# Kernel optimization log

Measured on AMD Instinct MI355X. Metric: run time of the kernel, lower is better.

Reference implementation:

```python
import jax, jax.numpy as jnp
import numpy as np
from jax import lax

BN_EPS = 1e-5


def _bn(t, g, b, m, v):
    # eval-mode BatchNorm2d over channel axis 1
    scale = (g / jnp.sqrt(v + BN_EPS))[None, :, None, None]
    return (t - m[None, :, None, None]) * scale + b[None, :, None, None]


def _conv1x1(t, w):
    # w: (out_c, in_c)
    return jnp.einsum('bchw,oc->bohw', t, w)


def setup_inputs() -> dict:
    key = jax.random.key(0)
    ks = jax.random.split(key, 8)
    B, C_in, H, W = 16, 640, 32, 32
    x = jax.random.normal(ks[0], (B, C_in, H, W), dtype=jnp.float32)

    def bn_params(k, c):
        k1, k2, k3, k4 = jax.random.split(k, 4)
        return (jax.random.normal(k1, (c,), jnp.float32) * 0.1 + 1.0,  # gamma
                jax.random.normal(k2, (c,), jnp.float32) * 0.1,        # beta
                jax.random.normal(k3, (c,), jnp.float32) * 0.1,        # running mean
                jax.random.uniform(k4, (c,), jnp.float32) + 0.5)       # running var

    bn1_g, bn1_b, bn1_m, bn1_v = bn_params(ks[1], 640)
    w_in = jax.random.normal(ks[2], (64, 640), jnp.float32) / np.sqrt(640)
    bnin_g, bnin_b, bnin_m, bnin_v = bn_params(ks[3], 64)
    w_emb = jax.random.normal(ks[4], (640, 1664), jnp.float32) / np.sqrt(1664)
    bne_g, bne_b, bne_m, bne_v = bn_params(ks[5], 640)
    w_out = jax.random.normal(ks[6], (640, 640), jnp.float32) / np.sqrt(640)
    bno_g, bno_b, bno_m, bno_v = bn_params(ks[7], 640)

    return dict(x=x,
                bn1_g=bn1_g, bn1_b=bn1_b, bn1_m=bn1_m, bn1_v=bn1_v,
                w_in=w_in, bnin_g=bnin_g, bnin_b=bnin_b, bnin_m=bnin_m, bnin_v=bnin_v,
                w_emb=w_emb, bne_g=bne_g, bne_b=bne_b, bne_m=bne_m, bne_v=bne_v,
                w_out=w_out, bno_g=bno_g, bno_b=bno_b, bno_m=bno_m, bno_v=bno_v)


def reference(x,
              bn1_g, bn1_b, bn1_m, bn1_v,
              w_in, bnin_g, bnin_b, bnin_m, bnin_v,
              w_emb, bne_g, bne_b, bne_m, bne_v,
              w_out, bno_g, bno_b, bno_m, bno_v):
    KH, KW = 5, 5
    x = jax.nn.relu(_bn(x, bn1_g, bn1_b, bn1_m, bn1_v))
    x = jax.nn.relu(_bn(_conv1x1(x, w_in), bnin_g, bnin_b, bnin_m, bnin_v))
    x0 = jax.nn.relu(x)  # second ReLU in original forward (no-op but faithful)
    # F.normalize(x, dim=1, p=2), eps=1e-12 (PyTorch default)
    norm = jnp.sqrt(jnp.sum(x0 * x0, axis=1, keepdims=True))
    identity = x0 / jnp.maximum(norm, 1e-12)
    b, c, h, w = identity.shape
    # unfold: (b, c*KH*KW, h, w), channel-major ordering matches torch Unfold
    patches = lax.conv_general_dilated_patches(
        identity, (KH, KW), (1, 1), ((2, 2), (2, 2)))
    corr = patches.reshape(b, c, KH * KW, h, w) * identity[:, :, None, :, :]
    corr = corr.reshape(b, c * KH * KW, h, w)
    # featureL2Norm: sqrt(sum(x^2, 1) + 1e-6)
    gs = corr / jnp.sqrt(jnp.sum(corr * corr, axis=1, keepdims=True) + 1e-6)
    feat = jnp.concatenate([identity, gs], axis=1)  # (b, 1664, h, w)
    e = jax.nn.relu(_bn(_conv1x1(feat, w_emb), bne_g, bne_b, bne_m, bne_v))
    out = _bn(_conv1x1(e, w_out), bno_g, bno_b, bno_m, bno_v)
    # dropout in eval mode = identity
    return out
```

## Files before the change

kernel.cpp:

```cpp
#include <hip/hip_runtime.h>
#include <math.h>

#define BN_EPS 1e-5f

using short8  = __attribute__((ext_vector_type(8))) short;
using f32x16  = __attribute__((ext_vector_type(16))) float;


__device__ __forceinline__ float bflo(unsigned u) { return __uint_as_float(u << 16); }
__device__ __forceinline__ float bfhi(unsigned u) { return __uint_as_float(u & 0xffff0000u); }

__device__ __forceinline__ unsigned bf16_rne(float f) {
    unsigned u = __float_as_uint(f);
    return (u + 0x7fffu + ((u >> 16) & 1u)) >> 16;
}
__device__ __forceinline__ unsigned pack_bf16(float lo, float hi) {
    return bf16_rne(lo) | (bf16_rne(hi) << 16);
}
__device__ __forceinline__ unsigned pk_hu(float lo, float hi) {
    unsigned a = __float_as_uint(lo) + 0x8000u;
    unsigned b = __float_as_uint(hi) + 0x8000u;
    return __builtin_amdgcn_perm(b, a, 0x07060302u);
}
__device__ __forceinline__ unsigned pmul_fast(unsigned a, unsigned b) {
    return pk_hu(bflo(a) * bflo(b), bfhi(a) * bfhi(b));
}

__global__ __launch_bounds__(256)
void k_prepAll(const float* __restrict__ g1, const float* __restrict__ b1,
               const float* __restrict__ m1, const float* __restrict__ v1,
               const float* __restrict__ w_in,
               const float* __restrict__ gi, const float* __restrict__ bi,
               const float* __restrict__ mi, const float* __restrict__ vi,
               const float* __restrict__ w_emb,
               const float* __restrict__ ge, const float* __restrict__ be,
               const float* __restrict__ me, const float* __restrict__ ve,
               const float* __restrict__ w_out,
               const float* __restrict__ go, const float* __restrict__ bo,
               const float* __restrict__ mo, const float* __restrict__ vo,
               float* __restrict__ s1, float* __restrict__ b1c,
               float* __restrict__ biasI, float* __restrict__ biasE, float* __restrict__ biasO,
               unsigned* __restrict__ wIt, unsigned* __restrict__ wEt, unsigned* __restrict__ wOt)
{
    __shared__ float row[1664];
    const int tid = threadIdx.x;

    if (blockIdx.x < 640) {
        const int oc = blockIdx.x;
#pragma unroll
        for (int it = 0; it < 2; it++) {
            int u = it * 256 + tid;
            if (u < 416)
                ((float4*)row)[u] = ((const float4*)&w_emb[(size_t)oc * 1664])[u];
        }
        __syncthreads();
        if (tid < 208) {
            int kc = tid >> 2, kh = (tid >> 1) & 1, ksub = tid & 1;
            int k0 = kc * 32 + kh * 16 + ksub * 8;
            float sc = ge[oc] * rsqrtf(ve[oc] + BN_EPS);
            float v[8];
#pragma unroll
            for (int j = 0; j < 8; j++) {
                int kgp = k0 + j;
                int orig;
                if (kgp < 64) orig = kgp;
                else { int t = kgp - 64; orig = 64 + (t & 63) * 25 + (t >> 6); }
                v[j] = row[orig] * sc;
            }
            int mt = oc >> 7, mf = (oc >> 5) & 3;
            int idx = (mt * 52 + kc) * 512 + (mf * 2 + kh) * 64 + ksub * 32 + (oc & 31);
            ((uint4*)wEt)[idx] = make_uint4(pack_bf16(v[0], v[1]), pack_bf16(v[2], v[3]),
                                            pack_bf16(v[4], v[5]), pack_bf16(v[6], v[7]));
        }
        return;
    }

    int i = (blockIdx.x - 640) * 256 + tid;

    if (i < 640) {
        float s = g1[i] * rsqrtf(v1[i] + BN_EPS);
        s1[i] = s; b1c[i] = b1[i] - m1[i] * s;
    } else if (i < 704) {
        int c = i - 640;
        float s = gi[c] * rsqrtf(vi[c] + BN_EPS);
        biasI[c] = bi[c] - mi[c] * s;
    } else if (i < 1344) {
        int c = i - 704;
        float s = ge[c] * rsqrtf(ve[c] + BN_EPS);
        biasE[c] = be[c] - me[c] * s;
    } else if (i < 1984) {
        int c = i - 1344;
        float s = go[c] * rsqrtf(vo[c] + BN_EPS);
        biasO[c] = bo[c] - mo[c] * s;
    }

    if (i >= 2048 && i < 7168) {
        int u = i - 2048;
        int kc = u >> 8, w = u & 255;
        int mf = w >> 7, kh = (w >> 6) & 1, sl = w & 63;
        int oc = mf * 32 + (sl & 31);
        int k0 = kc * 32 + kh * 16 + (sl >> 5) * 8;
        float sc = gi[oc] * rsqrtf(vi[oc] + BN_EPS);
        unsigned d[4];
#pragma unroll
        for (int q = 0; q < 4; q++)
            d[q] = pack_bf16(w_in[oc * 640 + k0 + 2 * q] * sc,
                             w_in[oc * 640 + k0 + 2 * q + 1] * sc);
        ((uint4*)wIt)[u] = make_uint4(d[0], d[1], d[2], d[3]);
    }

    if (i >= 8192 && i < 59392) {
        int u = i - 8192;
        int ci = u >> 9, w = u & 511;
        int mt = ci / 20, kc = ci - mt * 20;
        int mf = w >> 7, kh = (w >> 6) & 1, sl = w & 63;
        int oc = mt * 128 + mf * 32 + (sl & 31);
        int k0 = kc * 32 + kh * 16 + (sl >> 5) * 8;
        float sc = go[oc] * rsqrtf(vo[oc] + BN_EPS);
        unsigned d[4];
#pragma unroll
        for (int q = 0; q < 4; q++)
            d[q] = pack_bf16(w_out[oc * 640 + k0 + 2 * q] * sc,
                             w_out[oc * 640 + k0 + 2 * q + 1] * sc);
        ((uint4*)wOt)[u] = make_uint4(d[0], d[1], d[2], d[3]);
    }
}

__global__ __launch_bounds__(512, 1)
void k_identity(const float* __restrict__ x,
                const float* __restrict__ s1, const float* __restrict__ b1c,
                const unsigned* __restrict__ wIt, const float* __restrict__ biasI,
                unsigned* __restrict__ ident)
{
    __shared__ short smem[2][4096];
    __shared__ float Tpart[64 * 65];
    __shared__ float T[64 * 68];
    __shared__ float inv[64];

    const int tid  = threadIdx.x;
    const int half = tid >> 8;
    const int t    = tid & 255;
    const int l = t & 63, wv = t >> 6;
    const int mf = wv >> 1, nf = wv & 1;
    const int p0 = blockIdx.x * 64;
    const int b = p0 >> 10, hw0 = p0 & 1023;

    f32x16 acc;
#pragma unroll
    for (int r = 0; r < 16; r++) acc[r] = 0.f;

    for (int i = 0; i < 10; i++) {
        const int kc = half * 10 + i;
        uint4 av = ((const uint4*)wIt)[kc * 256 + t];
        int bnf = t >> 7, bkh = (t >> 6) & 1, sl = t & 63;
        int px = bnf * 32 + (sl & 31);
        int ch0 = kc * 32 + bkh * 16 + (sl >> 5) * 8;
        float4 sA = *(const float4*)&s1[ch0], sB = *(const float4*)&s1[ch0 + 4];
        float4 bA = *(const float4*)&b1c[ch0], bB = *(const float4*)&b1c[ch0 + 4];
        float vv[8];
        const float* xp = &x[((size_t)b * 640 + ch0) * 1024 + hw0 + px];
        vv[0] = fmaxf(fmaf(xp[0], sA.x, bA.x), 0.f);
        vv[1] = fmaxf(fmaf(xp[1024], sA.y, bA.y), 0.f);
        vv[2] = fmaxf(fmaf(xp[2048], sA.z, bA.z), 0.f);
        vv[3] = fmaxf(fmaf(xp[3072], sA.w, bA.w), 0.f);
        vv[4] = fmaxf(fmaf(xp[4096], sB.x, bB.x), 0.f);
        vv[5] = fmaxf(fmaf(xp[5120], sB.y, bB.y), 0.f);
        vv[6] = fmaxf(fmaf(xp[6144], sB.z, bB.z), 0.f);
        vv[7] = fmaxf(fmaf(xp[7168], sB.w, bB.w), 0.f);
        uint4 bvpk = make_uint4(pack_bf16(vv[0], vv[1]), pack_bf16(vv[2], vv[3]),
                                pack_bf16(vv[4], vv[5]), pack_bf16(vv[6], vv[7]));
        __syncthreads();
        ((uint4*)smem[half])[t] = av;
        ((uint4*)(smem[half] + 2048))[t] = bvpk;
        __syncthreads();
#pragma unroll
        for (int kh = 0; kh < 2; kh++) {
            short8 a  = *(const short8*)&smem[half][((mf * 2 + kh) * 64 + l) * 8];
            short8 bb = *(const short8*)&smem[half][2048 + ((nf * 2 + kh) * 64 + l) * 8];
            acc = __builtin_amdgcn_mfma_f32_32x32x16_bf16(a, bb, acc, 0, 0, 0);
        }
    }
    if (half == 1) {
#pragma unroll
        for (int r = 0; r < 16; r++) {
            int m = mf * 32 + (r & 3) + 8 * (r >> 2) + 4 * (l >> 5);
            int px = nf * 32 + (l & 31);
            Tpart[px * 65 + m] = acc[r];
        }
    }
    __syncthreads();
    if (half == 0) {
#pragma unroll
        for (int r = 0; r < 16; r++) {
            int m = mf * 32 + (r & 3) + 8 * (r >> 2) + 4 * (l >> 5);
            int px = nf * 32 + (l & 31);
            float v = acc[r] + Tpart[px * 65 + m];
            T[px * 68 + m] = fmaxf(v + biasI[m], 0.f);
        }
    }
    __syncthreads();
    if (tid < 64) {
        float sum = 0.f;
#pragma unroll 8
        for (int c = 0; c < 64; c++) { float v = T[tid * 68 + c]; sum = fmaf(v, v, sum); }
        inv[tid] = 1.f / fmaxf(sqrtf(sum), 1e-12f);
    }
    __syncthreads();
    {
        int px = tid >> 3, q = tid & 7;
        float iv = inv[px];
        unsigned d[4];
#pragma unroll
        for (int t2 = 0; t2 < 4; t2++)
            d[t2] = pack_bf16(T[px * 68 + q * 8 + 2 * t2] * iv,
                              T[px * 68 + q * 8 + 2 * t2 + 1] * iv);
        *(uint4*)&ident[(size_t)(p0 + px) * 32 + q * 4] = make_uint4(d[0], d[1], d[2], d[3]);
    }
}

__device__ __forceinline__ uint4 gen_feat_unit(const short* slab, const short* ctrs,
                                               int kcAbs, int t)
{
    const int hf = t >> 7, sl = t & 63;
    const int bkh = (t >> 6) & 1;
    const int cl = bkh * 16 + (sl >> 5) * 8;
    if (kcAbs < 2) {
        int spxC = (hf + 2) * 36 + (sl & 31) + 2;
        return *(const uint4*)&slab[spxC * 72 + kcAbs * 32 + cl];
    } else {
        int pxl = hf * 32 + (sl & 31);
        int idx = kcAbs - 2;
        int ksp = idx >> 1;
        int cb = (idx & 1) * 32 + cl;
        int kho = ksp / 5, kwo = ksp - kho * 5;
        int spx = (hf + kho) * 36 + (sl & 31) + kwo;
        const unsigned* nb = (const unsigned*)&slab[spx * 72 + cb];
        const unsigned* ct = (const unsigned*)&ctrs[pxl * 72 + cb];
        return make_uint4(pmul_fast(nb[0], ct[0]), pmul_fast(nb[1], ct[1]),
                          pmul_fast(nb[2], ct[2]), pmul_fast(nb[3], ct[3]));
    }
}

__global__ __launch_bounds__(640, 1)
void k_fused(const unsigned* __restrict__ ident,
             const unsigned* __restrict__ wEt, const float* __restrict__ biasE,
             const unsigned* __restrict__ wOt, const float* __restrict__ biasO,
             float* __restrict__ out)
{
    __shared__ short slab[15552];
    __shared__ short ctrs[4608];
    __shared__ float invDs[64];
    __shared__ char  stg[2][16384];
    __shared__ uint4 Ep[20 * 256];

    const int tid = threadIdx.x;
    const int l = tid & 63;
    const int w = tid >> 6;
    const int mt = w >> 1, mf0 = (w & 1) * 2;
    const int pt = blockIdx.x;
    const int b = pt >> 4, r0 = (pt & 15) * 2;

#pragma unroll
    for (int it = 0; it < 3; it++) {
        int u = it * 640 + tid;
        if (u < 1728) {
            int spx = u >> 3, q = u & 7;
            int sr = spx / 36, sc = spx - sr * 36;
            int r = r0 + sr - 2, cc = sc - 2;
            uint4 v = make_uint4(0u, 0u, 0u, 0u);
            if (r >= 0 && r < 32 && cc >= 0 && cc < 32)
                v = *(const uint4*)&ident[((size_t)(b * 1024 + r * 32 + cc) * 64 + q * 8) / 2];
            *(uint4*)&slab[spx * 72 + q * 8] = v;
        }
    }
    __syncthreads();

    if (tid < 512) {
        int px = tid >> 3, part = tid & 7;
        int rh = px >> 5, rw = px & 31;
        float ctr[8];
        const unsigned* cp = (const unsigned*)&slab[((rh + 2) * 36 + rw + 2) * 72 + part * 8];
#pragma unroll
        for (int d = 0; d < 4; d++) { ctr[2 * d] = bflo(cp[d]); ctr[2 * d + 1] = bfhi(cp[d]); }
        float sum = 0.f;
#pragma unroll
        for (int k = 0; k < 25; k++) {
            const int kh = k / 5, kw = k % 5;
            const unsigned* nb = (const unsigned*)&slab[((rh + kh) * 36 + rw + kw) * 72 + part * 8];
#pragma unroll
            for (int d = 0; d < 4; d++) {
                float q0 = bflo(nb[d]) * ctr[2 * d];
                float q1 = bfhi(nb[d]) * ctr[2 * d + 1];
                sum = fmaf(q0, q0, sum); sum = fmaf(q1, q1, sum);
            }
        }
        sum += __shfl_xor(sum, 1);
        sum += __shfl_xor(sum, 2);
        sum += __shfl_xor(sum, 4);
        if (part == 0) invDs[px] = rsqrtf(sum + 1e-6f);
    }
    __syncthreads();

    if (tid < 512) {
        int px = tid >> 3, q = tid & 7;
        int spx = ((px >> 5) + 2) * 36 + (px & 31) + 2;
        const unsigned* src = (const unsigned*)&slab[spx * 72 + q * 8];
        float iv = invDs[px];
        unsigned d[4];
#pragma unroll
        for (int dd = 0; dd < 4; dd++)
            d[dd] = pk_hu(bflo(src[dd]) * iv, bfhi(src[dd]) * iv);
        *(uint4*)&ctrs[px * 72 + q * 8] = make_uint4(d[0], d[1], d[2], d[3]);
    }
    __syncthreads();

    const uint4* A = (const uint4*)wEt + (size_t)(mt * 52) * 512;
    const bool has2 = (tid < 384);

    f32x16 acc[2][2];
#pragma unroll
    for (int i = 0; i < 2; i++)
#pragma unroll
        for (int j = 0; j < 2; j++)
#pragma unroll
            for (int r = 0; r < 16; r++) acc[i][j][r] = 0.f;

    {
        uint4 f = gen_feat_unit(slab, ctrs, (tid >> 8), tid & 255);
        *(uint4*)&stg[0][tid * 16] = f;
        if (has2) {
            int u = tid + 640;
            uint4 f2 = gen_feat_unit(slab, ctrs, (u >> 8), u & 255);
            *(uint4*)&stg[0][u * 16] = f2;
        }
    }
    __syncthreads();

    for (int c = 0; c < 13; c++) {
        const int cur = c & 1, nxt = cur ^ 1;
        if (c < 12) {
            int kc0 = (c + 1) * 4;
            uint4 f = gen_feat_unit(slab, ctrs, kc0 + (tid >> 8), tid & 255);
            *(uint4*)&stg[nxt][tid * 16] = f;
            if (has2) {
                int u = tid + 640;
                uint4 f2 = gen_feat_unit(slab, ctrs, kc0 + (u >> 8), u & 255);
                *(uint4*)&stg[nxt][u * 16] = f2;
            }
        }
#pragma unroll
        for (int kcL = 0; kcL < 4; kcL++) {
            const int kc = c * 4 + kcL;
            uint4 av[2][2], bv[2][2];
#pragma unroll
            for (int mi = 0; mi < 2; mi++)
#pragma unroll
                for (int kh = 0; kh < 2; kh++)
                    av[mi][kh] = A[(size_t)kc * 512 + (((mf0 + mi) * 2 + kh) << 6) + l];
#pragma unroll
            for (int ni = 0; ni < 2; ni++)
#pragma unroll
                for (int kh = 0; kh < 2; kh++)
                    bv[ni][kh] = *(const uint4*)&stg[cur][(kcL * 256 + (ni << 7) + (kh << 6) + l) * 16];
#pragma unroll
            for (int kh = 0; kh < 2; kh++) {
                acc[0][0] = __builtin_amdgcn_mfma_f32_32x32x16_bf16(*(short8*)&av[0][kh], *(short8*)&bv[0][kh], acc[0][0], 0, 0, 0);
                acc[0][1] = __builtin_amdgcn_mfma_f32_32x32x16_bf16(*(short8*)&av[0][kh], *(short8*)&bv[1][kh], acc[0][1], 0, 0, 0);
                acc[1][0] = __builtin_amdgcn_mfma_f32_32x32x16_bf16(*(short8*)&av[1][kh], *(short8*)&bv[0][kh], acc[1][0], 0, 0, 0);
                acc[1][1] = __builtin_amdgcn_mfma_f32_32x32x16_bf16(*(short8*)&av[1][kh], *(short8*)&bv[1][kh], acc[1][1], 0, 0, 0);
            }
        }
        __syncthreads();
    }

#pragma unroll
    for (int mi = 0; mi < 2; mi++) {
        const int kbase = (w * 2 + mi) * 256;
#pragma unroll
        for (int ni = 0; ni < 2; ni++) {
#pragma unroll
            for (int rg = 0; rg < 4; rg++) {
                int ocb = w * 64 + mi * 32 + 8 * rg + 4 * (l >> 5);
                float4 bb = *(const float4*)&biasE[ocb];
                unsigned d0 = pack_bf16(fmaxf(acc[mi][ni][rg * 4 + 0] + bb.x, 0.f),
                                        fmaxf(acc[mi][ni][rg * 4 + 1] + bb.y, 0.f));
                unsigned d1 = pack_bf16(fmaxf(acc[mi][ni][rg * 4 + 2] + bb.z, 0.f),
                                        fmaxf(acc[mi][ni][rg * 4 + 3] + bb.w, 0.f));
                int unit = kbase + (ni << 7) + ((rg >> 1) << 6) + ((rg & 1) << 5) + (l & 31);
                ((uint2*)Ep)[unit * 2 + (l >> 5)] = make_uint2(d0, d1);
            }
        }
    }
    __syncthreads();

    const int p0 = pt * 64;
    const int hw0 = p0 & 1023;
    const uint4* Ao = (const uint4*)wOt + (size_t)(mt * 20) * 512;

    f32x16 acc2[2][2];
#pragma unroll
    for (int i = 0; i < 2; i++)
#pragma unroll
        for (int j = 0; j < 2; j++)
#pragma unroll
            for (int r = 0; r < 16; r++) acc2[i][j][r] = 0.f;

#pragma unroll 2
    for (int kc = 0; kc < 20; kc++) {
        uint4 av[2][2], bv[2][2];
#pragma unroll
        for (int mi = 0; mi < 2; mi++)
#pragma unroll
            for (int kh = 0; kh < 2; kh++)
                av[mi][kh] = Ao[(size_t)kc * 512 + (((mf0 + mi) * 2 + kh) << 6) + l];
#pragma unroll
        for (int ni = 0; ni < 2; ni++)
#pragma unroll
            for (int kh = 0; kh < 2; kh++)
                bv[ni][kh] = Ep[kc * 256 + (ni << 7) + (kh << 6) + l];
#pragma unroll
        for (int kh = 0; kh < 2; kh++) {
            acc2[0][0] = __builtin_amdgcn_mfma_f32_32x32x16_bf16(*(short8*)&av[0][kh], *(short8*)&bv[0][kh], acc2[0][0], 0, 0, 0);
            acc2[0][1] = __builtin_amdgcn_mfma_f32_32x32x16_bf16(*(short8*)&av[0][kh], *(short8*)&bv[1][kh], acc2[0][1], 0, 0, 0);
            acc2[1][0] = __builtin_amdgcn_mfma_f32_32x32x16_bf16(*(short8*)&av[1][kh], *(short8*)&bv[0][kh], acc2[1][0], 0, 0, 0);
            acc2[1][1] = __builtin_amdgcn_mfma_f32_32x32x16_bf16(*(short8*)&av[1][kh], *(short8*)&bv[1][kh], acc2[1][1], 0, 0, 0);
        }
    }

#pragma unroll
    for (int mi = 0; mi < 2; mi++)
#pragma unroll
        for (int ni = 0; ni < 2; ni++) {
            int pxl = ni * 32 + (l & 31);
#pragma unroll
            for (int r = 0; r < 16; r++) {
                int oc = w * 64 + mi * 32 + (r & 3) + 8 * (r >> 2) + 4 * (l >> 5);
                out[((size_t)b * 640 + oc) * 1024 + hw0 + pxl] = acc2[mi][ni][r] + biasO[oc];
            }
        }
}

extern "C" void kernel_launch(void* const* d_in, const int* in_sizes, int n_in,
                              void* d_out, int out_size, void* d_ws, size_t ws_size,
                              hipStream_t stream)
{
    const float* x    = (const float*)d_in[0];
    const float* g1   = (const float*)d_in[1];
    const float* b1   = (const float*)d_in[2];
    const float* m1   = (const float*)d_in[3];
    const float* v1   = (const float*)d_in[4];
    const float* w_in = (const float*)d_in[5];
    const float* gi   = (const float*)d_in[6];
    const float* bi   = (const float*)d_in[7];
    const float* mi   = (const float*)d_in[8];
    const float* vi   = (const float*)d_in[9];
    const float* w_emb= (const float*)d_in[10];
    const float* ge   = (const float*)d_in[11];
    const float* be   = (const float*)d_in[12];
    const float* me   = (const float*)d_in[13];
    const float* ve   = (const float*)d_in[14];
    const float* w_out= (const float*)d_in[15];
    const float* go   = (const float*)d_in[16];
    const float* bo   = (const float*)d_in[17];
    const float* mo   = (const float*)d_in[18];
    const float* vo   = (const float*)d_in[19];

    char* ws = (char*)d_ws;
    float*    s1    = (float*)(ws + 0);
    float*    b1c   = (float*)(ws + 2560);
    float*    biasI = (float*)(ws + 5120);
    float*    biasE = (float*)(ws + 5376);
    float*    biasO = (float*)(ws + 7936);
    unsigned* wIt   = (unsigned*)(ws + 16384);
    unsigned* wOt   = (unsigned*)(ws + 98304);
    unsigned* wEt   = (unsigned*)(ws + 917504);
    unsigned* ident = (unsigned*)(ws + 3047424);
    float*    out   = (float*)d_out;

    k_prepAll<<<872, 256, 0, stream>>>(g1, b1, m1, v1, w_in, gi, bi, mi, vi,
                                       w_emb, ge, be, me, ve, w_out, go, bo, mo, vo,
                                       s1, b1c, biasI, biasE, biasO, wIt, wEt, wOt);
    k_identity<<<256, 512, 0, stream>>>(x, s1, b1c, wIt, biasI, ident);
    k_fused<<<256, 640, 0, stream>>>(ident, wEt, biasE, wOt, biasO, out);
}
```

Before: 195.6 us.

## Halve fused-kernel pixel tile to one row, doubling grid to 512 blocks

The fused correlation+embedding+output kernel now processes one image row (32 pixels) per block instead of two rows, launching 512 blocks. Shared memory and accumulators shrink, and launch bounds allow several blocks per CU. This targets the MI355X's 256 CUs being only one block deep, trading better occupancy and latency hiding for halved weight reuse (each weight tile is read twice as often) and higher halo overhead in the slab load.

```diff
diff --git a/kernel.cpp b/kernel.cpp
--- a/kernel.cpp
+++ b/kernel.cpp
@@ -218,52 +218,51 @@
     }
 }
 
-__device__ __forceinline__ uint4 gen_feat_unit(const short* slab, const short* ctrs,
-                                               int kcAbs, int t)
+__device__ __forceinline__ uint4 gen_feat_unit32(const short* slab, const short* ctrs,
+                                                 int kcAbs, int t)
 {
-    const int hf = t >> 7, sl = t & 63;
+    const int sl = t & 63;
     const int bkh = (t >> 6) & 1;
+    const int px = sl & 31;
     const int cl = bkh * 16 + (sl >> 5) * 8;
     if (kcAbs < 2) {
-        int spxC = (hf + 2) * 36 + (sl & 31) + 2;
-        return *(const uint4*)&slab[spxC * 72 + kcAbs * 32 + cl];
+        return *(const uint4*)&slab[(2 * 36 + px + 2) * 72 + kcAbs * 32 + cl];
     } else {
-        int pxl = hf * 32 + (sl & 31);
         int idx = kcAbs - 2;
         int ksp = idx >> 1;
         int cb = (idx & 1) * 32 + cl;
         int kho = ksp / 5, kwo = ksp - kho * 5;
-        int spx = (hf + kho) * 36 + (sl & 31) + kwo;
+        int spx = kho * 36 + px + kwo;
         const unsigned* nb = (const unsigned*)&slab[spx * 72 + cb];
-        const unsigned* ct = (const unsigned*)&ctrs[pxl * 72 + cb];
+        const unsigned* ct = (const unsigned*)&ctrs[px * 72 + cb];
         return make_uint4(pmul_fast(nb[0], ct[0]), pmul_fast(nb[1], ct[1]),
                           pmul_fast(nb[2], ct[2]), pmul_fast(nb[3], ct[3]));
     }
 }
 
-__global__ __launch_bounds__(640, 1)
+__global__ __launch_bounds__(640, 5)
 void k_fused(const unsigned* __restrict__ ident,
              const unsigned* __restrict__ wEt, const float* __restrict__ biasE,
              const unsigned* __restrict__ wOt, const float* __restrict__ biasO,
              float* __restrict__ out)
 {
-    __shared__ short slab[15552];
-    __shared__ short ctrs[4608];
-    __shared__ float invDs[64];
-    __shared__ char  stg[2][16384];
-    __shared__ uint4 Ep[20 * 256];
+    __shared__ short slab[180 * 72];
+    __shared__ short ctrs[32 * 72];
+    __shared__ float invDs[32];
+    __shared__ char  stg[2][4096];
+    __shared__ uint4 Ep[20 * 128];
 
     const int tid = threadIdx.x;
     const int l = tid & 63;
     const int w = tid >> 6;
     const int mt = w >> 1, mf0 = (w & 1) * 2;
-    const int pt = blockIdx.x;
-    const int b = pt >> 4, r0 = (pt & 15) * 2;
+    const int b = blockIdx.x >> 5;
+    const int r0 = blockIdx.x & 31;
 
 #pragma unroll
     for (int it = 0; it < 3; it++) {
         int u = it * 640 + tid;
-        if (u < 1728) {
+        if (u < 1440) {
             int spx = u >> 3, q = u & 7;
             int sr = spx / 36, sc = spx - sr * 36;
             int r = r0 + sr - 2, cc = sc - 2;
@@ -275,18 +274,17 @@
     }
     __syncthreads();
 
-    if (tid < 512) {
+    if (tid < 256) {
         int px = tid >> 3, part = tid & 7;
-        int rh = px >> 5, rw = px & 31;
         float ctr[8];
-        const unsigned* cp = (const unsigned*)&slab[((rh + 2) * 36 + rw + 2) * 72 + part * 8];
+        const unsigned* cp = (const unsigned*)&slab[(2 * 36 + px + 2) * 72 + part * 8];
 #pragma unroll
         for (int d = 0; d < 4; d++) { ctr[2 * d] = bflo(cp[d]); ctr[2 * d + 1] = bfhi(cp[d]); }
         float sum = 0.f;
 #pragma unroll
         for (int k = 0; k < 25; k++) {
             const int kh = k / 5, kw = k % 5;
-            const unsigned* nb = (const unsigned*)&slab[((rh + kh) * 36 + rw + kw) * 72 + part * 8];
+            const unsigned* nb = (const unsigned*)&slab[(kh * 36 + px + kw) * 72 + part * 8];
 #pragma unroll
             for (int d = 0; d < 4; d++) {
                 float q0 = bflo(nb[d]) * ctr[2 * d];
@@ -301,10 +299,9 @@
     }
     __syncthreads();
 
-    if (tid < 512) {
+    if (tid < 256) {
         int px = tid >> 3, q = tid & 7;
-        int spx = ((px >> 5) + 2) * 36 + (px & 31) + 2;
-        const unsigned* src = (const unsigned*)&slab[spx * 72 + q * 8];
+        const unsigned* src = (const unsigned*)&slab[(2 * 36 + px + 2) * 72 + q * 8];
         float iv = invDs[px];
         unsigned d[4];
 #pragma unroll
@@ -315,59 +312,42 @@
     __syncthreads();
 
     const uint4* A = (const uint4*)wEt + (size_t)(mt * 52) * 512;
-    const bool has2 = (tid < 384);
-
-    f32x16 acc[2][2];
+
+    f32x16 acc[2];
 #pragma unroll
     for (int i = 0; i < 2; i++)
 #pragma unroll
-        for (int j = 0; j < 2; j++)
-#pragma unroll
-            for (int r = 0; r < 16; r++) acc[i][j][r] = 0.f;
-
-    {
-        uint4 f = gen_feat_unit(slab, ctrs, (tid >> 8), tid & 255);
+        for (int r = 0; r < 16; r++) acc[i][r] = 0.f;
+
+    if (tid < 256) {
+        uint4 f = gen_feat_unit32(slab, ctrs, tid >> 7, tid & 127);
         *(uint4*)&stg[0][tid * 16] = f;
-        if (has2) {
-            int u = tid + 640;
-            uint4 f2 = gen_feat_unit(slab, ctrs, (u >> 8), u & 255);
-            *(uint4*)&stg[0][u * 16] = f2;
-        }
-    }
-    __syncthreads();
-
-    for (int c = 0; c < 13; c++) {
+    }
+    __syncthreads();
+
+    for (int c = 0; c < 26; c++) {
         const int cur = c & 1, nxt = cur ^ 1;
-        if (c < 12) {
-            int kc0 = (c + 1) * 4;
-            uint4 f = gen_feat_unit(slab, ctrs, kc0 + (tid >> 8), tid & 255);
+        if (c < 25 && tid < 256) {
+            int kc0 = (c + 1) * 2;
+            uint4 f = gen_feat_unit32(slab, ctrs, kc0 + (tid >> 7), tid & 127);
             *(uint4*)&stg[nxt][tid * 16] = f;
-            if (has2) {
-                int u = tid + 640;
-                uint4 f2 = gen_feat_unit(slab, ctrs, kc0 + (u >> 8), u & 255);
-                *(uint4*)&stg[nxt][u * 16] = f2;
-            }
-        }
-#pragma unroll
-        for (int kcL = 0; kcL < 4; kcL++) {
-            const int kc = c * 4 + kcL;
-            uint4 av[2][2], bv[2][2];
+        }
+#pragma unroll
+        for (int kcL = 0; kcL < 2; kcL++) {
+            const int kc = c * 2 + kcL;
+            uint4 av[2][2], bv[2];
 #pragma unroll
             for (int mi = 0; mi < 2; mi++)
 #pragma unroll
                 for (int kh = 0; kh < 2; kh++)
                     av[mi][kh] = A[(size_t)kc * 512 + (((mf0 + mi) * 2 + kh) << 6) + l];
 #pragma unroll
-            for (int ni = 0; ni < 2; ni++)
-#pragma unroll
-                for (int kh = 0; kh < 2; kh++)
-                    bv[ni][kh] = *(const uint4*)&stg[cur][(kcL * 256 + (ni << 7) + (kh << 6) + l) * 16];
+            for (int kh = 0; kh < 2; kh++)
+                bv[kh] = *(const uint4*)&stg[cur][(kcL * 128 + (kh << 6) + l) * 16];
 #pragma unroll
             for (int kh = 0; kh < 2; kh++) {
-                acc[0][0] = __builtin_amdgcn_mfma_f32_32x32x16_bf16(*(short8*)&av[0][kh], *(short8*)&bv[0][kh], acc[0][0], 0, 0, 0);
-                acc[0][1] = __builtin_amdgcn_mfma_f32_32x32x16_bf16(*(short8*)&av[0][kh], *(short8*)&bv[1][kh], acc[0][1], 0, 0, 0);
-                acc[1][0] = __builtin_amdgcn_mfma_f32_32x32x16_bf16(*(short8*)&av[1][kh], *(short8*)&bv[0][kh], acc[1][0], 0, 0, 0);
-                acc[1][1] = __builtin_amdgcn_mfma_f32_32x32x16_bf16(*(short8*)&av[1][kh], *(short8*)&bv[1][kh], acc[1][1], 0, 0, 0);
+                acc[0] = __builtin_amdgcn_mfma_f32_32x32x16_bf16(*(short8*)&av[0][kh], *(short8*)&bv[kh], acc[0], 0, 0, 0);
+                acc[1] = __builtin_amdgcn_mfma_f32_32x32x16_bf16(*(short8*)&av[1][kh], *(short8*)&bv[kh], acc[1], 0, 0, 0);
             }
         }
         __syncthreads();
@@ -375,69 +355,57 @@
 
 #pragma unroll
     for (int mi = 0; mi < 2; mi++) {
-        const int kbase = (w * 2 + mi) * 256;
-#pragma unroll
-        for (int ni = 0; ni < 2; ni++) {
-#pragma unroll
-            for (int rg = 0; rg < 4; rg++) {
-                int ocb = w * 64 + mi * 32 + 8 * rg + 4 * (l >> 5);
-                float4 bb = *(const float4*)&biasE[ocb];
-                unsigned d0 = pack_bf16(fmaxf(acc[mi][ni][rg * 4 + 0] + bb.x, 0.f),
-                                        fmaxf(acc[mi][ni][rg * 4 + 1] + bb.y, 0.f));
-                unsigned d1 = pack_bf16(fmaxf(acc[mi][ni][rg * 4 + 2] + bb.z, 0.f),
-                                        fmaxf(acc[mi][ni][rg * 4 + 3] + bb.w, 0.f));
-                int unit = kbase + (ni << 7) + ((rg >> 1) << 6) + ((rg & 1) << 5) + (l & 31);
-                ((uint2*)Ep)[unit * 2 + (l >> 5)] = make_uint2(d0, d1);
-            }
-        }
-    }
-    __syncthreads();
-
-    const int p0 = pt * 64;
-    const int hw0 = p0 & 1023;
+        const int kbase = (w * 2 + mi) * 128;
+#pragma unroll
+        for (int rg = 0; rg < 4; rg++) {
+            int ocb = w * 64 + mi * 32 + 8 * rg + 4 * (l >> 5);
+            float4 bb = *(const float4*)&biasE[ocb];
+            unsigned d0 = pack_bf16(fmaxf(acc[mi][rg * 4 + 0] + bb.x, 0.f),
+                                    fmaxf(acc[mi][rg * 4 + 1] + bb.y, 0.f));
+            unsigned d1 = pack_bf16(fmaxf(acc[mi][rg * 4 + 2] + bb.z, 0.f),
+                                    fmaxf(acc[mi][rg * 4 + 3] + bb.w, 0.f));
+            int unit = kbase + ((rg >> 1) << 6) + ((rg & 1) << 5) + (l & 31);
+            ((uint2*)Ep)[unit * 2 + (l >> 5)] = make_uint2(d0, d1);
+        }
+    }
+    __syncthreads();
+
+    const int hw0 = r0 * 32;
     const uint4* Ao = (const uint4*)wOt + (size_t)(mt * 20) * 512;
 
-    f32x16 acc2[2][2];
+    f32x16 acc2[2];
 #pragma unroll
     for (int i = 0; i < 2; i++)
 #pragma unroll
-        for (int j = 0; j < 2; j++)
-#pragma unroll
-            for (int r = 0; r < 16; r++) acc2[i][j][r] = 0.f;
+        for (int r = 0; r < 16; r++) acc2[i][r] = 0.f;
 
 #pragma unroll 2
     for (int kc = 0; kc < 20; kc++) {
-        uint4 av[2][2], bv[2][2];
+        uint4 av[2][2], bv[2];
 #pragma unroll
         for (int mi = 0; mi < 2; mi++)
 #pragma unroll
             for (int kh = 0; kh < 2; kh++)
                 av[mi][kh] = Ao[(size_t)kc * 512 + (((mf0 + mi) * 2 + kh) << 6) + l];
 #pragma unroll
-        for (int ni = 0; ni < 2; ni++)
-#pragma unroll
-            for (int kh = 0; kh < 2; kh++)
-                bv[ni][kh] = Ep[kc * 256 + (ni << 7) + (kh << 6) + l];
+        for (int kh = 0; kh < 2; kh++)
+            bv[kh] = Ep[kc * 128 + (kh << 6) + l];
 #pragma unroll
         for (int kh = 0; kh < 2; kh++) {
-            acc2[0][0] = __builtin_amdgcn_mfma_f32_32x32x16_bf16(*(short8*)&av[0][kh], *(short8*)&bv[0][kh], acc2[0][0], 0, 0, 0);
-            acc2[0][1] = __builtin_amdgcn_mfma_f32_32x32x16_bf16(*(short8*)&av[0][kh], *(short8*)&bv[1][kh], acc2[0][1], 0, 0, 0);
-            acc2[1][0] = __builtin_amdgcn_mfma_f32_32x32x16_bf16(*(short8*)&av[1][kh], *(short8*)&bv[0][kh], acc2[1][0], 0, 0, 0);
-            acc2[1][1] = __builtin_amdgcn_mfma_f32_32x32x16_bf16(*(short8*)&av[1][kh], *(short8*)&bv[1][kh], acc2[1][1], 0, 0, 0);
-        }
-    }
-
-#pragma unroll
-    for (int mi = 0; mi < 2; mi++)
-#pragma unroll
-        for (int ni = 0; ni < 2; ni++) {
-            int pxl = ni * 32 + (l & 31);
-#pragma unroll
-            for (int r = 0; r < 16; r++) {
-                int oc = w * 64 + mi * 32 + (r & 3) + 8 * (r >> 2) + 4 * (l >> 5);
-                out[((size_t)b * 640 + oc) * 1024 + hw0 + pxl] = acc2[mi][ni][r] + biasO[oc];
-            }
-        }
+            acc2[0] = __builtin_amdgcn_mfma_f32_32x32x16_bf16(*(short8*)&av[0][kh], *(short8*)&bv[kh], acc2[0], 0, 0, 0);
+            acc2[1] = __builtin_amdgcn_mfma_f32_32x32x16_bf16(*(short8*)&av[1][kh], *(short8*)&bv[kh], acc2[1], 0, 0, 0);
+        }
+    }
+
+#pragma unroll
+    for (int mi = 0; mi < 2; mi++) {
+        int px = l & 31;
+#pragma unroll
+        for (int r = 0; r < 16; r++) {
+            int oc = w * 64 + mi * 32 + (r & 3) + 8 * (r >> 2) + 4 * (l >> 5);
+            out[((size_t)b * 640 + oc) * 1024 + hw0 + px] = acc2[mi][r] + biasO[oc];
+        }
+    }
 }
 
 extern "C" void kernel_launch(void* const* d_in, const int* in_sizes, int n_in,
@@ -481,5 +449,5 @@
                                        w_emb, ge, be, me, ve, w_out, go, bo, mo, vo,
                                        s1, b1c, biasI, biasE, biasO, wIt, wEt, wOt);
     k_identity<<<256, 512, 0, stream>>>(x, s1, b1c, wIt, biasI, ident);
-    k_fused<<<256, 640, 0, stream>>>(ident, wEt, biasE, wOt, biasO, out);
-}
+    k_fused<<<512, 640, 0, stream>>>(ident, wEt, biasE, wOt, biasO, out);
+}
```

After: 221.8 us. 1.13x slower.

## Fuse identity computation into main kernel with halo recompute

Applied to the files above, without the earlier changes.

Removes the separate k_identity kernel and the ident buffer round-trip. Each block of the fused kernel now computes BN+ReLU, the 640->64 conv, ReLU and L2 normalization for its 216-pixel halo slab directly from x using MFMA, and writes the result into shared memory. This saves one launch and the global write/read of the intermediate, but recomputes halo rows (216 vs 64 pixels per block, roughly 3.4x the identity work) and reads x with strided per-channel loads. Launch bounds were also changed to request 3 waves per EU.

```diff
diff --git a/kernel.cpp b/kernel.cpp
--- a/kernel.cpp
+++ b/kernel.cpp
@@ -123,98 +123,6 @@
             d[q] = pack_bf16(w_out[oc * 640 + k0 + 2 * q] * sc,
                              w_out[oc * 640 + k0 + 2 * q + 1] * sc);
         ((uint4*)wOt)[u] = make_uint4(d[0], d[1], d[2], d[3]);
-    }
-}
-
-__global__ __launch_bounds__(512, 1)
-void k_identity(const float* __restrict__ x,
-                const float* __restrict__ s1, const float* __restrict__ b1c,
-                const unsigned* __restrict__ wIt, const float* __restrict__ biasI,
-                unsigned* __restrict__ ident)
-{
-    __shared__ short smem[2][4096];
-    __shared__ float Tpart[64 * 65];
-    __shared__ float T[64 * 68];
-    __shared__ float inv[64];
-
-    const int tid  = threadIdx.x;
-    const int half = tid >> 8;
-    const int t    = tid & 255;
-    const int l = t & 63, wv = t >> 6;
-    const int mf = wv >> 1, nf = wv & 1;
-    const int p0 = blockIdx.x * 64;
-    const int b = p0 >> 10, hw0 = p0 & 1023;
-
-    f32x16 acc;
-#pragma unroll
-    for (int r = 0; r < 16; r++) acc[r] = 0.f;
-
-    for (int i = 0; i < 10; i++) {
-        const int kc = half * 10 + i;
-        uint4 av = ((const uint4*)wIt)[kc * 256 + t];
-        int bnf = t >> 7, bkh = (t >> 6) & 1, sl = t & 63;
-        int px = bnf * 32 + (sl & 31);
-        int ch0 = kc * 32 + bkh * 16 + (sl >> 5) * 8;
-        float4 sA = *(const float4*)&s1[ch0], sB = *(const float4*)&s1[ch0 + 4];
-        float4 bA = *(const float4*)&b1c[ch0], bB = *(const float4*)&b1c[ch0 + 4];
-        float vv[8];
-        const float* xp = &x[((size_t)b * 640 + ch0) * 1024 + hw0 + px];
-        vv[0] = fmaxf(fmaf(xp[0], sA.x, bA.x), 0.f);
-        vv[1] = fmaxf(fmaf(xp[1024], sA.y, bA.y), 0.f);
-        vv[2] = fmaxf(fmaf(xp[2048], sA.z, bA.z), 0.f);
-        vv[3] = fmaxf(fmaf(xp[3072], sA.w, bA.w), 0.f);
-        vv[4] = fmaxf(fmaf(xp[4096], sB.x, bB.x), 0.f);
-        vv[5] = fmaxf(fmaf(xp[5120], sB.y, bB.y), 0.f);
-        vv[6] = fmaxf(fmaf(xp[6144], sB.z, bB.z), 0.f);
-        vv[7] = fmaxf(fmaf(xp[7168], sB.w, bB.w), 0.f);
-        uint4 bvpk = make_uint4(pack_bf16(vv[0], vv[1]), pack_bf16(vv[2], vv[3]),
-                                pack_bf16(vv[4], vv[5]), pack_bf16(vv[6], vv[7]));
-        __syncthreads();
-        ((uint4*)smem[half])[t] = av;
-        ((uint4*)(smem[half] + 2048))[t] = bvpk;
-        __syncthreads();
-#pragma unroll
-        for (int kh = 0; kh < 2; kh++) {
-            short8 a  = *(const short8*)&smem[half][((mf * 2 + kh) * 64 + l) * 8];
-            short8 bb = *(const short8*)&smem[half][2048 + ((nf * 2 + kh) * 64 + l) * 8];
-            acc = __builtin_amdgcn_mfma_f32_32x32x16_bf16(a, bb, acc, 0, 0, 0);
-        }
-    }
-    if (half == 1) {
-#pragma unroll
-        for (int r = 0; r < 16; r++) {
-            int m = mf * 32 + (r & 3) + 8 * (r >> 2) + 4 * (l >> 5);
-            int px = nf * 32 + (l & 31);
-            Tpart[px * 65 + m] = acc[r];
-        }
-    }
-    __syncthreads();
-    if (half == 0) {
-#pragma unroll
-        for (int r = 0; r < 16; r++) {
-            int m = mf * 32 + (r & 3) + 8 * (r >> 2) + 4 * (l >> 5);
-            int px = nf * 32 + (l & 31);
-            float v = acc[r] + Tpart[px * 65 + m];
-            T[px * 68 + m] = fmaxf(v + biasI[m], 0.f);
-        }
-    }
-    __syncthreads();
-    if (tid < 64) {
-        float sum = 0.f;
-#pragma unroll 8
-        for (int c = 0; c < 64; c++) { float v = T[tid * 68 + c]; sum = fmaf(v, v, sum); }
-        inv[tid] = 1.f / fmaxf(sqrtf(sum), 1e-12f);
-    }
-    __syncthreads();
-    {
-        int px = tid >> 3, q = tid & 7;
-        float iv = inv[px];
-        unsigned d[4];
-#pragma unroll
-        for (int t2 = 0; t2 < 4; t2++)
-            d[t2] = pack_bf16(T[px * 68 + q * 8 + 2 * t2] * iv,
-                              T[px * 68 + q * 8 + 2 * t2 + 1] * iv);
-        *(uint4*)&ident[(size_t)(p0 + px) * 32 + q * 4] = make_uint4(d[0], d[1], d[2], d[3]);
     }
 }
 
@@ -241,14 +149,16 @@
     }
 }
 
-__global__ __launch_bounds__(640, 1)
-void k_fused(const unsigned* __restrict__ ident,
-             const unsigned* __restrict__ wEt, const float* __restrict__ biasE,
-             const unsigned* __restrict__ wOt, const float* __restrict__ biasO,
-             float* __restrict__ out)
+__global__ __launch_bounds__(640, 3)
+void k_mega(const float* __restrict__ x,
+            const float* __restrict__ s1, const float* __restrict__ b1c,
+            const unsigned* __restrict__ wIt, const float* __restrict__ biasI,
+            const unsigned* __restrict__ wEt, const float* __restrict__ biasE,
+            const unsigned* __restrict__ wOt, const float* __restrict__ biasO,
+            float* __restrict__ out)
 {
-    __shared__ short slab[15552];
-    __shared__ short ctrs[4608];
+    __shared__ short slab[216 * 72];
+    __shared__ short ctrs[64 * 72];
     __shared__ float invDs[64];
     __shared__ char  stg[2][16384];
     __shared__ uint4 Ep[20 * 256];
@@ -260,17 +170,77 @@
     const int pt = blockIdx.x;
     const int b = pt >> 4, r0 = (pt & 15) * 2;
 
-#pragma unroll
-    for (int it = 0; it < 3; it++) {
-        int u = it * 640 + tid;
-        if (u < 1728) {
-            int spx = u >> 3, q = u & 7;
-            int sr = spx / 36, sc = spx - sr * 36;
-            int r = r0 + sr - 2, cc = sc - 2;
-            uint4 v = make_uint4(0u, 0u, 0u, 0u);
-            if (r >= 0 && r < 32 && cc >= 0 && cc < 32)
-                v = *(const uint4*)&ident[((size_t)(b * 1024 + r * 32 + cc) * 64 + q * 8) / 2];
-            *(uint4*)&slab[spx * 72 + q * 8] = v;
+    if (w < 7) {
+        const int spx = w * 32 + (l & 31);
+        const int spxc = spx < 216 ? spx : 215;
+        const int sr = spxc / 36, sc = spxc - sr * 36;
+        const int r = r0 + sr - 2, cc = sc - 2;
+        const bool valid = (spx < 216) && (r >= 0) && (r < 32) && (cc >= 0) && (cc < 32);
+        const int rcl = min(max(r, 0), 31), ccl = min(max(cc, 0), 31);
+        const float* xp = x + (size_t)b * 655360 + (size_t)(rcl * 32 + ccl);
+        const float vm = valid ? 1.f : 0.f;
+
+        f32x16 accI[2];
+#pragma unroll
+        for (int i = 0; i < 2; i++)
+#pragma unroll
+            for (int rr = 0; rr < 16; rr++) accI[i][rr] = 0.f;
+
+        for (int kc = 0; kc < 20; kc++) {
+            uint4 av[2][2];
+#pragma unroll
+            for (int mi2 = 0; mi2 < 2; mi2++)
+#pragma unroll
+                for (int kh = 0; kh < 2; kh++)
+                    av[mi2][kh] = ((const uint4*)wIt)[kc * 256 + (mi2 << 7) + (kh << 6) + l];
+#pragma unroll
+            for (int kh = 0; kh < 2; kh++) {
+                const int ch0 = kc * 32 + kh * 16 + (l >> 5) * 8;
+                float4 sA = *(const float4*)&s1[ch0], sB = *(const float4*)&s1[ch0 + 4];
+                float4 bA = *(const float4*)&b1c[ch0], bB = *(const float4*)&b1c[ch0 + 4];
+                const float* xc = xp + (size_t)ch0 * 1024;
+                float vv[8];
+                vv[0] = fmaxf(fmaf(xc[0],    sA.x, bA.x), 0.f) * vm;
+                vv[1] = fmaxf(fmaf(xc[1024], sA.y, bA.y), 0.f) * vm;
+                vv[2] = fmaxf(fmaf(xc[2048], sA.z, bA.z), 0.f) * vm;
+                vv[3] = fmaxf(fmaf(xc[3072], sA.w, bA.w), 0.f) * vm;
+                vv[4] = fmaxf(fmaf(xc[4096], sB.x, bB.x), 0.f) * vm;
+                vv[5] = fmaxf(fmaf(xc[5120], sB.y, bB.y), 0.f) * vm;
+                vv[6] = fmaxf(fmaf(xc[6144], sB.z, bB.z), 0.f) * vm;
+                vv[7] = fmaxf(fmaf(xc[7168], sB.w, bB.w), 0.f) * vm;
+                unsigned bu[4] = { pack_bf16(vv[0], vv[1]), pack_bf16(vv[2], vv[3]),
+                                   pack_bf16(vv[4], vv[5]), pack_bf16(vv[6], vv[7]) };
+                short8 bf = *(short8*)bu;
+                accI[0] = __builtin_amdgcn_mfma_f32_32x32x16_bf16(*(short8*)&av[0][kh], bf, accI[0], 0, 0, 0);
+                accI[1] = __builtin_amdgcn_mfma_f32_32x32x16_bf16(*(short8*)&av[1][kh], bf, accI[1], 0, 0, 0);
+            }
+        }
+        float ss = 0.f;
+#pragma unroll
+        for (int mi2 = 0; mi2 < 2; mi2++)
+#pragma unroll
+            for (int rg = 0; rg < 4; rg++) {
+                float4 bb = *(const float4*)&biasI[mi2 * 32 + 8 * rg + 4 * (l >> 5)];
+#pragma unroll
+                for (int q = 0; q < 4; q++) {
+                    float bv = (q == 0) ? bb.x : (q == 1) ? bb.y : (q == 2) ? bb.z : bb.w;
+                    float t = fmaxf(accI[mi2][rg * 4 + q] + bv, 0.f);
+                    accI[mi2][rg * 4 + q] = t;
+                    ss = fmaf(t, t, ss);
+                }
+            }
+        ss += __shfl_xor(ss, 32);
+        float inv = 1.f / fmaxf(sqrtf(ss), 1e-12f);
+        if (spx < 216) {
+#pragma unroll
+            for (int mi2 = 0; mi2 < 2; mi2++)
+#pragma unroll
+                for (int rg = 0; rg < 4; rg++) {
+                    unsigned d0 = pack_bf16(accI[mi2][rg * 4 + 0] * inv, accI[mi2][rg * 4 + 1] * inv);
+                    unsigned d1 = pack_bf16(accI[mi2][rg * 4 + 2] * inv, accI[mi2][rg * 4 + 3] * inv);
+                    if (!valid) { d0 = 0u; d1 = 0u; }
+                    *(uint2*)&slab[spx * 72 + mi2 * 32 + 8 * rg + 4 * (l >> 5)] = make_uint2(d0, d1);
+                }
         }
     }
     __syncthreads();
@@ -474,12 +444,11 @@
     unsigned* wIt   = (unsigned*)(ws + 16384);
     unsigned* wOt   = (unsigned*)(ws + 98304);
     unsigned* wEt   = (unsigned*)(ws + 917504);
-    unsigned* ident = (unsigned*)(ws + 3047424);
     float*    out   = (float*)d_out;
 
     k_prepAll<<<872, 256, 0, stream>>>(g1, b1, m1, v1, w_in, gi, bi, mi, vi,
                                        w_emb, ge, be, me, ve, w_out, go, bo, mo, vo,
                                        s1, b1c, biasI, biasE, biasO, wIt, wEt, wOt);
-    k_identity<<<256, 512, 0, stream>>>(x, s1, b1c, wIt, biasI, ident);
-    k_fused<<<256, 640, 0, stream>>>(ident, wEt, biasE, wOt, biasO, out);
-}
+    k_mega<<<256, 640, 0, stream>>>(x, s1, b1c, wIt, biasI,
+                                    wEt, biasE, wOt, biasO, out);
+}
```

Measured after the change: 196.2 us. No clear change (+0.3%).
